# Performance work log

Hardware: AMD Instinct MI355X
Metric: run time of the kernel (lower is better)

## Reference

```python
import jax, jax.numpy as jnp
import numpy as np

N = 1048576          # number of sample points
C = 32               # feature_dim per plane
PAIRS = ((0, 1), (0, 2), (1, 2))  # itertools.combinations(range(3), 2)


def setup_inputs() -> dict:
    key = jax.random.key(0)
    k0, k1, k2, k3 = jax.random.split(key, 4)
    # grid_sample coords must lie in [-1, 1]
    x = jax.random.uniform(k0, (N, 3), jnp.float32, -1.0, 1.0)
    # torch.nn.init.uniform_ default is U[0, 1)
    planes_128 = jax.random.uniform(k1, (3, C, 128, 128), jnp.float32)
    planes_256 = jax.random.uniform(k2, (3, C, 256, 256), jnp.float32)
    planes_512 = jax.random.uniform(k3, (3, C, 512, 512), jnp.float32)
    return {"x": x, "planes_128": planes_128, "planes_256": planes_256,
            "planes_512": planes_512}


def _bilinear_sample(plane, coords):
    """plane: (C, H, W); coords: (N, 2) in [-1,1], last dim = (x, y).
    Matches torch grid_sample(mode='bilinear', align_corners=True).
    Returns (N, C)."""
    _, H, W = plane.shape
    gx, gy = coords[:, 0], coords[:, 1]
    ix = (gx + 1.0) * 0.5 * (W - 1)   # x indexes width
    iy = (gy + 1.0) * 0.5 * (H - 1)   # y indexes height
    x0f = jnp.clip(jnp.floor(ix), 0.0, W - 1)
    y0f = jnp.clip(jnp.floor(iy), 0.0, H - 1)
    wx = ix - x0f
    wy = iy - y0f
    x0 = x0f.astype(jnp.int32)
    y0 = y0f.astype(jnp.int32)
    x1 = jnp.minimum(x0 + 1, W - 1)
    y1 = jnp.minimum(y0 + 1, H - 1)
    v00 = plane[:, y0, x0]  # (C, N)
    v01 = plane[:, y0, x1]
    v10 = plane[:, y1, x0]
    v11 = plane[:, y1, x1]
    out = (v00 * (1 - wx) * (1 - wy) + v01 * wx * (1 - wy)
           + v10 * (1 - wx) * wy + v11 * wx * wy)  # (C, N)
    return out.T  # (N, C)


def reference(x, planes_128, planes_256, planes_512):
    # coords[p] = x[:, (i, j)] for pair p -> grid (x=dim i, y=dim j)
    coords = jnp.stack([x[:, jnp.array(p)] for p in PAIRS])  # (3, N, 2)
    feats = []
    for planes in (planes_128, planes_256, planes_512):
        sampled = jax.vmap(_bilinear_sample)(planes, coords)  # (3, N, C)
        feats.append(jnp.prod(sampled, axis=0))               # (N, C)
    return jnp.concatenate(feats, axis=-1)  # (N, 96); dropout(p=0) is identity
```

## Files before the change

### kernel.cpp

```cpp
#include <hip/hip_runtime.h>
#include <hip/hip_fp16.h>


constexpr int kN = 1048576;
constexpr int kC = 32;
constexpr int kCells = 32 * 32 * 32;

typedef float f32x4 __attribute__((ext_vector_type(4)));
typedef short s16x4 __attribute__((ext_vector_type(4)));

__global__ __launch_bounds__(1024) void kp_transpose_h(const float* __restrict__ in,
                                                       __half* __restrict__ out, int R) {
    __shared__ float tile[32][33];
    const int tx = threadIdx.x, ty = threadIdx.y;
    const int x0 = blockIdx.x * 32;
    const int y  = blockIdx.y;
    const int p  = blockIdx.z;
    tile[ty][tx] = in[(((size_t)p * kC + ty) * R + y) * R + x0 + tx];
    __syncthreads();
    out[(((size_t)p * R + y) * R + x0 + ty) * kC + tx] = __float2half_rn(tile[tx][ty]);
}

__device__ __forceinline__ unsigned cell_key(float x, float y, float z) {
    int cx = min(max((int)((x + 1.f) * 16.f), 0), 31);
    int cy = min(max((int)((y + 1.f) * 16.f), 0), 31);
    int cz = min(max((int)((z + 1.f) * 16.f), 0), 31);
    unsigned m = 0;
#pragma unroll
    for (int b = 0; b < 5; ++b) {
        m |= ((unsigned)((cx >> b) & 1)) << (3 * b);
        m |= ((unsigned)((cy >> b) & 1)) << (3 * b + 1);
        m |= ((unsigned)((cz >> b) & 1)) << (3 * b + 2);
    }
    return m;
}

__global__ __launch_bounds__(256) void kp_zero(unsigned* __restrict__ p, int n) {
    int i = blockIdx.x * 256 + threadIdx.x;
    if (i < n) p[i] = 0u;
}

__global__ __launch_bounds__(256) void kp_hist(const float* __restrict__ xs,
                                               unsigned* __restrict__ hist) {
    int n = blockIdx.x * 256 + threadIdx.x;
    float x = xs[n * 3 + 0], y = xs[n * 3 + 1], z = xs[n * 3 + 2];
    atomicAdd(&hist[cell_key(x, y, z)], 1u);
}

__global__ __launch_bounds__(1024) void kp_scan(const unsigned* __restrict__ hist,
                                                unsigned* __restrict__ cursor) {
    __shared__ unsigned sums[1024];
    const int t = threadIdx.x;
    const int per = kCells / 1024;
    unsigned local[32];
    unsigned s = 0;
    const int base = t * per;
#pragma unroll
    for (int i = 0; i < per; ++i) { local[i] = hist[base + i]; s += local[i]; }
    sums[t] = s;
    __syncthreads();
    for (int off = 1; off < 1024; off <<= 1) {
        unsigned v = (t >= off) ? sums[t - off] : 0u;
        __syncthreads();
        sums[t] += v;
        __syncthreads();
    }
    unsigned run = (t == 0) ? 0u : sums[t - 1];
#pragma unroll
    for (int i = 0; i < per; ++i) { cursor[base + i] = run; run += local[i]; }
}

__global__ __launch_bounds__(256) void kp_scatter(const float* __restrict__ xs,
                                                  unsigned* __restrict__ cursor,
                                                  f32x4* __restrict__ sorted) {
    int n = blockIdx.x * 256 + threadIdx.x;
    float x = xs[n * 3 + 0], y = xs[n * 3 + 1], z = xs[n * 3 + 2];
    unsigned pos = atomicAdd(&cursor[cell_key(x, y, z)], 1u);
    f32x4 v = {x, y, z, __uint_as_float((unsigned)n)};
    __builtin_nontemporal_store(v, &sorted[pos]);
}

__device__ __forceinline__ void cvt4(const s16x4& s, float* v) {
    union { s16x4 s; __half2 h[2]; } u;
    u.s = s;
    float2 f01 = __half22float2(u.h[0]);
    float2 f23 = __half22float2(u.h[1]);
    v[0] = f01.x; v[1] = f01.y; v[2] = f23.x; v[3] = f23.y;
}

__global__ __launch_bounds__(256, 4) void kp_sample_sorted(const f32x4* __restrict__ pts,
                                                           const __half* __restrict__ planes,
                                                           float* __restrict__ out) {
    constexpr unsigned offr[3] = {0u,
                                  3u * 128 * 128 * 32,
                                  3u * 128 * 128 * 32 + 3u * 256 * 256 * 32};
    const int nwg = (kN * 8) / 256;
    int bid = blockIdx.x;
    bid = (bid & 7) * (nwg / 8) + (bid >> 3);
    const int li = threadIdx.x;
    const int n  = bid * 32 + (li >> 3);
    const unsigned c4 = (li & 7) << 2;
    f32x4 pt = pts[n];
    const float a = pt.x, b = pt.y, d = pt.z;
    const unsigned oi = __float_as_uint(pt.w);
    const float gx[3] = {a, a, b};
    const float gy[3] = {b, d, d};

    s16x4 v00[9], v01[9], v10[9], v11[9];
    float wxa[9], wya[9];
#pragma unroll
    for (int q = 0; q < 9; ++q) {
        const int r = q / 3, p = q % 3;
        const int R = 128 << r;
        const float fr = (float)(R - 1);
        float ix = (gx[p] + 1.f) * 0.5f * fr;
        float iy = (gy[p] + 1.f) * 0.5f * fr;
        float x0f = fminf(fmaxf(floorf(ix), 0.f), fr);
        float y0f = fminf(fmaxf(floorf(iy), 0.f), fr);
        wxa[q] = ix - x0f;
        wya[q] = iy - y0f;
        unsigned xi0 = (unsigned)x0f, yi0 = (unsigned)y0f;
        unsigned xi1 = min(xi0 + 1u, (unsigned)(R - 1));
        unsigned yi1 = min(yi0 + 1u, (unsigned)(R - 1));
        unsigned pb = offr[r] + (unsigned)p * (unsigned)(R * R) * 32u + c4;
        unsigned r0 = pb + yi0 * (unsigned)R * 32u;
        unsigned r1 = pb + yi1 * (unsigned)R * 32u;
        v00[q] = *reinterpret_cast<const s16x4*>(planes + r0 + xi0 * 32u);
        v01[q] = *reinterpret_cast<const s16x4*>(planes + r0 + xi1 * 32u);
        v10[q] = *reinterpret_cast<const s16x4*>(planes + r1 + xi0 * 32u);
        v11[q] = *reinterpret_cast<const s16x4*>(planes + r1 + xi1 * 32u);
    }
    float* o = out + (size_t)oi * 96 + c4;
#pragma unroll
    for (int r = 0; r < 3; ++r) {
        float f[4] = {1.f, 1.f, 1.f, 1.f};
#pragma unroll
        for (int p = 0; p < 3; ++p) {
            const int q = r * 3 + p;
            const float wx = wxa[q], wy = wya[q];
            const float w00 = (1.f - wx) * (1.f - wy), w01 = wx * (1.f - wy);
            const float w10 = (1.f - wx) * wy,         w11 = wx * wy;
            float a00[4], a01[4], a10[4], a11[4];
            cvt4(v00[q], a00); cvt4(v01[q], a01);
            cvt4(v10[q], a10); cvt4(v11[q], a11);
#pragma unroll
            for (int j = 0; j < 4; ++j)
                f[j] *= w00 * a00[j] + w01 * a01[j] + w10 * a10[j] + w11 * a11[j];
        }
        __builtin_nontemporal_store(f32x4{f[0], f[1], f[2], f[3]}, (f32x4*)(o + r * 32));
    }
}

__global__ __launch_bounds__(256) void kp_sample_f32(const float* __restrict__ xs,
                                                     const float* __restrict__ p128,
                                                     const float* __restrict__ p256,
                                                     const float* __restrict__ p512,
                                                     float* __restrict__ out) {
    const int t = blockIdx.x * 256 + (int)threadIdx.x;
    const int n = t >> 5;
    const int c = t & 31;
    const float a = xs[n * 3 + 0], b = xs[n * 3 + 1], d = xs[n * 3 + 2];
    const float gxs[3] = {a, a, b};
    const float gys[3] = {b, d, d};
    const float* planes[3] = {p128, p256, p512};
    const int Rs[3] = {128, 256, 512};
    float* o = out + (size_t)n * 96;
#pragma unroll
    for (int r = 0; r < 3; ++r) {
        const int R = Rs[r];
        const float fr = (float)(R - 1);
        float f = 1.0f;
#pragma unroll
        for (int p = 0; p < 3; ++p) {
            float ix = (gxs[p] + 1.f) * 0.5f * fr;
            float iy = (gys[p] + 1.f) * 0.5f * fr;
            float x0f = fminf(fmaxf(floorf(ix), 0.f), fr);
            float y0f = fminf(fmaxf(floorf(iy), 0.f), fr);
            float wx = ix - x0f, wy = iy - y0f;
            int xi0 = (int)x0f, yi0 = (int)y0f;
            int xi1 = min(xi0 + 1, R - 1), yi1 = min(yi0 + 1, R - 1);
            const float* pc = planes[r] + ((size_t)p * kC + c) * R * R;
            float v00 = pc[yi0 * R + xi0], v01 = pc[yi0 * R + xi1];
            float v10 = pc[yi1 * R + xi0], v11 = pc[yi1 * R + xi1];
            f *= v00 * (1.f - wx) * (1.f - wy) + v01 * wx * (1.f - wy)
               + v10 * (1.f - wx) * wy + v11 * wx * wy;
        }
        __builtin_nontemporal_store(f, o + r * 32 + c);
    }
}

extern "C" void kernel_launch(void* const* d_in, const int* in_sizes, int n_in,
                              void* d_out, int out_size, void* d_ws, size_t ws_size,
                              hipStream_t stream) {
    const float* xs   = (const float*)d_in[0];
    const float* p128 = (const float*)d_in[1];
    const float* p256 = (const float*)d_in[2];
    const float* p512 = (const float*)d_in[3];
    float* out = (float*)d_out;

    const size_t n128 = (size_t)3 * 128 * 128 * kC;
    const size_t n256 = (size_t)3 * 256 * 256 * kC;
    const size_t n512 = (size_t)3 * 512 * 512 * kC;
    const size_t planes_b = (n128 + n256 + n512) * sizeof(__half);
    const size_t sorted_b = (size_t)kN * 16;
    const size_t hist_b   = (size_t)kCells * 4;
    const size_t need = sorted_b + planes_b + 2 * hist_b + 256;

    dim3 tblk(32, 32);
    const int nblk8 = (kN * 8) / 256;

    if (ws_size >= need) {
        f32x4* sorted = (f32x4*)d_ws;
        __half* t128 = (__half*)((char*)d_ws + sorted_b);
        __half* t256 = t128 + n128;
        __half* t512 = t256 + n256;
        unsigned* hist   = (unsigned*)((char*)d_ws + sorted_b + planes_b);
        unsigned* cursor = hist + kCells;

        kp_transpose_h<<<dim3(128 / 32, 128, 3), tblk, 0, stream>>>(p128, t128, 128);
        kp_transpose_h<<<dim3(256 / 32, 256, 3), tblk, 0, stream>>>(p256, t256, 256);
        kp_transpose_h<<<dim3(512 / 32, 512, 3), tblk, 0, stream>>>(p512, t512, 512);
        kp_zero<<<(kCells + 255) / 256, 256, 0, stream>>>(hist, kCells);
        kp_hist<<<kN / 256, 256, 0, stream>>>(xs, hist);
        kp_scan<<<1, 1024, 0, stream>>>(hist, cursor);
        kp_scatter<<<kN / 256, 256, 0, stream>>>(xs, cursor, sorted);
        kp_sample_sorted<<<nblk8, 256, 0, stream>>>(sorted, t128, out);
    } else {
        kp_sample_f32<<<(kN * 32) / 256, 256, 0, stream>>>(xs, p128, p256, p512, out);
    }
}
```

Measured before the change: 395.3 us.

## Load adjacent bilinear columns with 16-byte loads and combine via lane shuffle

Each bilinear sample now issues two 16-byte loads, one per row, instead of four 8-byte corner loads. This relies on the x0 and x0+1 columns being contiguous in the channels-last fp16 layout: half of each 8-lane group reads column x0 and the other half reads column x0+1. Each lane blends its two rows in y, scales by its own x weight, and an xor-shuffle across the two halves sums the x contributions. The sampling loop is also restructured so loads and math are interleaved per resolution, and the min-waves launch-bounds hint is dropped. The x1 clamp is gone, so at the last column the load reads past the row end. That value gets zero weight, but at the very end of the last plane it reads beyond the buffer.

```diff
diff --git a/kernel.cpp b/kernel.cpp
--- a/kernel.cpp
+++ b/kernel.cpp
@@ -7,7 +7,7 @@
 constexpr int kCells = 32 * 32 * 32;
 
 typedef float f32x4 __attribute__((ext_vector_type(4)));
-typedef short s16x4 __attribute__((ext_vector_type(4)));
+typedef short s16x8 __attribute__((ext_vector_type(8)));
 
 __global__ __launch_bounds__(1024) void kp_transpose_h(const float* __restrict__ in,
                                                        __half* __restrict__ out, int R) {
@@ -80,17 +80,9 @@
     __builtin_nontemporal_store(v, &sorted[pos]);
 }
 
-__device__ __forceinline__ void cvt4(const s16x4& s, float* v) {
-    union { s16x4 s; __half2 h[2]; } u;
-    u.s = s;
-    float2 f01 = __half22float2(u.h[0]);
-    float2 f23 = __half22float2(u.h[1]);
-    v[0] = f01.x; v[1] = f01.y; v[2] = f23.x; v[3] = f23.y;
-}
-
-__global__ __launch_bounds__(256, 4) void kp_sample_sorted(const f32x4* __restrict__ pts,
-                                                           const __half* __restrict__ planes,
-                                                           float* __restrict__ out) {
+__global__ __launch_bounds__(256) void kp_sample_sorted(const f32x4* __restrict__ pts,
+                                                        const __half* __restrict__ planes,
+                                                        float* __restrict__ out) {
     constexpr unsigned offr[3] = {0u,
                                   3u * 128 * 128 * 32,
                                   3u * 128 * 128 * 32 + 3u * 256 * 256 * 32};
@@ -98,56 +90,55 @@
     int bid = blockIdx.x;
     bid = (bid & 7) * (nwg / 8) + (bid >> 3);
     const int li = threadIdx.x;
-    const int n  = bid * 32 + (li >> 3);
-    const unsigned c4 = (li & 7) << 2;
+    const int n    = bid * 32 + (li >> 3);
+    const int l    = li & 7;
+    const int side = l >> 2;
+    const int s    = l & 3;
     f32x4 pt = pts[n];
     const float a = pt.x, b = pt.y, d = pt.z;
     const unsigned oi = __float_as_uint(pt.w);
     const float gx[3] = {a, a, b};
     const float gy[3] = {b, d, d};
-
-    s16x4 v00[9], v01[9], v10[9], v11[9];
-    float wxa[9], wya[9];
-#pragma unroll
-    for (int q = 0; q < 9; ++q) {
-        const int r = q / 3, p = q % 3;
+    float* o = out + (size_t)oi * 96 + s * 8 + side * 4;
+
+#pragma unroll
+    for (int r = 0; r < 3; ++r) {
         const int R = 128 << r;
         const float fr = (float)(R - 1);
-        float ix = (gx[p] + 1.f) * 0.5f * fr;
-        float iy = (gy[p] + 1.f) * 0.5f * fr;
-        float x0f = fminf(fmaxf(floorf(ix), 0.f), fr);
-        float y0f = fminf(fmaxf(floorf(iy), 0.f), fr);
-        wxa[q] = ix - x0f;
-        wya[q] = iy - y0f;
-        unsigned xi0 = (unsigned)x0f, yi0 = (unsigned)y0f;
-        unsigned xi1 = min(xi0 + 1u, (unsigned)(R - 1));
-        unsigned yi1 = min(yi0 + 1u, (unsigned)(R - 1));
-        unsigned pb = offr[r] + (unsigned)p * (unsigned)(R * R) * 32u + c4;
-        unsigned r0 = pb + yi0 * (unsigned)R * 32u;
-        unsigned r1 = pb + yi1 * (unsigned)R * 32u;
-        v00[q] = *reinterpret_cast<const s16x4*>(planes + r0 + xi0 * 32u);
-        v01[q] = *reinterpret_cast<const s16x4*>(planes + r0 + xi1 * 32u);
-        v10[q] = *reinterpret_cast<const s16x4*>(planes + r1 + xi0 * 32u);
-        v11[q] = *reinterpret_cast<const s16x4*>(planes + r1 + xi1 * 32u);
-    }
-    float* o = out + (size_t)oi * 96 + c4;
-#pragma unroll
-    for (int r = 0; r < 3; ++r) {
-        float f[4] = {1.f, 1.f, 1.f, 1.f};
+        float prod[4] = {1.f, 1.f, 1.f, 1.f};
 #pragma unroll
         for (int p = 0; p < 3; ++p) {
-            const int q = r * 3 + p;
-            const float wx = wxa[q], wy = wya[q];
-            const float w00 = (1.f - wx) * (1.f - wy), w01 = wx * (1.f - wy);
-            const float w10 = (1.f - wx) * wy,         w11 = wx * wy;
-            float a00[4], a01[4], a10[4], a11[4];
-            cvt4(v00[q], a00); cvt4(v01[q], a01);
-            cvt4(v10[q], a10); cvt4(v11[q], a11);
-#pragma unroll
-            for (int j = 0; j < 4; ++j)
-                f[j] *= w00 * a00[j] + w01 * a01[j] + w10 * a10[j] + w11 * a11[j];
+            float ix = (gx[p] + 1.f) * 0.5f * fr;
+            float iy = (gy[p] + 1.f) * 0.5f * fr;
+            float x0f = fminf(fmaxf(floorf(ix), 0.f), fr);
+            float y0f = fminf(fmaxf(floorf(iy), 0.f), fr);
+            float wx = ix - x0f, wy = iy - y0f;
+            unsigned xi0 = (unsigned)x0f, yi0 = (unsigned)y0f;
+            unsigned yi1 = min(yi0 + 1u, (unsigned)(R - 1));
+            const __half* pb = planes + offr[r] + (size_t)p * R * R * 32u
+                             + (size_t)xi0 * 32u + (unsigned)l * 8u;
+            union U { s16x8 v; __half2 h[4]; } A, B;
+            A.v = *reinterpret_cast<const s16x8*>(pb + (size_t)yi0 * R * 32u);
+            B.v = *reinterpret_cast<const s16x8*>(pb + (size_t)yi1 * R * 32u);
+            const float xw = side ? wx : (1.f - wx);
+            float part[8];
+#pragma unroll
+            for (int j = 0; j < 4; ++j) {
+                float2 fa = __half22float2(A.h[j]);
+                float2 fb = __half22float2(B.h[j]);
+                part[2 * j]     = (fa.x + wy * (fb.x - fa.x)) * xw;
+                part[2 * j + 1] = (fa.y + wy * (fb.y - fa.y)) * xw;
+            }
+            const int j0 = side * 4;
+#pragma unroll
+            for (int j = 0; j < 8; ++j) {
+                float other = __shfl_xor(part[j], 4);
+                if (j >= j0 && j < j0 + 4)
+                    prod[j - j0] *= part[j] + other;
+            }
         }
-        __builtin_nontemporal_store(f32x4{f[0], f[1], f[2], f[3]}, (f32x4*)(o + r * 32));
+        __builtin_nontemporal_store(f32x4{prod[0], prod[1], prod[2], prod[3]},
+                                    (f32x4*)(o + r * 32));
     }
 }
 
```

New measurement: 553.1 us. 39.9% more time.
